# Performance work log

Measured on AMD Instinct MI355X. Metric: run time of the kernel, lower is better.

## Reference

```python
import jax, jax.numpy as jnp
import numpy as np

B_SZ = 8
G = 2048
D_MODEL = 512
D_STATE = 128
D_CONV = 4
EXPAND = 2
HEADDIM = 64
D_INNER = EXPAND * D_MODEL          # 1024
NHEADS = D_INNER // HEADDIM         # 16
CONV_DIM = D_INNER + 2 * D_STATE    # 1280
D_IN_PROJ = 2 * D_INNER + 2 * D_STATE + NHEADS  # 2320
ID_DIM = 128
CHR_DIM = 64
N_CHR = 25
F_LOCUS = 32
PATH_DIM = 128
GENE_FEAT = ID_DIM + PATH_DIM + 2 * CHR_DIM  # 384
N_PERT = 10000
P_DIM = 128


def silu(x):
    return x * jax.nn.sigmoid(x)


def causal_dw_conv(x, w, b):
    # x: (B,L,C), w: (C,K), b: (C,)  causal depthwise conv (left pad K-1)
    K = w.shape[1]
    L = x.shape[1]
    xp = jnp.pad(x, ((0, 0), (K - 1, 0), (0, 0)))
    out = b[None, None, :]
    for k in range(K):
        out = out + xp[:, k:k + L, :] * w[:, k][None, None, :]
    return out


def mamba2(u, in_w, conv_w, conv_b, dt_bias, A_log, Dp, norm_w, out_w):
    # u: (B,L,d_model) -> (B,L,d_model); mamba_ssm Mamba2 defaults, ngroups=1
    Bb, L, _ = u.shape
    zxbcdt = u @ in_w.T                                   # (B,L,D_IN_PROJ)
    z = zxbcdt[..., :D_INNER]
    xBC = zxbcdt[..., D_INNER:D_INNER + CONV_DIM]
    dt = zxbcdt[..., D_INNER + CONV_DIM:]                 # (B,L,H)
    xBC = silu(causal_dw_conv(xBC, conv_w, conv_b))
    x = xBC[..., :D_INNER].reshape(Bb, L, NHEADS, HEADDIM)
    Bm = xBC[..., D_INNER:D_INNER + D_STATE]              # (B,L,N)
    Cm = xBC[..., D_INNER + D_STATE:]                     # (B,L,N)
    dt = jax.nn.softplus(dt + dt_bias)                    # (B,L,H)
    dA = jnp.exp(dt * (-jnp.exp(A_log)))                  # (B,L,H)

    def step(h, inp):
        dA_t, dt_t, B_t, C_t, x_t = inp
        h = dA_t[:, :, None, None] * h + jnp.einsum('bh,bn,bhp->bhpn', dt_t, B_t, x_t)
        y = jnp.einsum('bhpn,bn->bhp', h, C_t)
        return h, y

    h0 = jnp.zeros((Bb, NHEADS, HEADDIM, D_STATE), u.dtype)
    xs = (dA.transpose(1, 0, 2), dt.transpose(1, 0, 2),
          Bm.transpose(1, 0, 2), Cm.transpose(1, 0, 2), x.transpose(1, 0, 2, 3))
    _, ys = jax.lax.scan(step, h0, xs)                    # ys: (L,B,H,P)
    y = ys.transpose(1, 0, 2, 3) + Dp[None, None, :, None] * x
    y = y.reshape(Bb, L, D_INNER)
    # gated RMSNorm (norm_before_gate=False): norm(y * silu(z))
    y = y * silu(z)
    y = y * jax.lax.rsqrt(jnp.mean(y * y, axis=-1, keepdims=True) + 1e-5) * norm_w
    return y @ out_w.T


def setup_inputs() -> dict:
    key = jax.random.key(0)
    ks = iter(jax.random.split(key, 48))

    def nrm(shape, scale):
        return jax.random.normal(next(ks), shape, jnp.float32) * scale

    inp = {}
    inp['perturbation_idx'] = jax.random.randint(next(ks), (B_SZ,), 0, N_PERT)
    inp['chr_idx'] = jax.random.randint(next(ks), (G,), 0, N_CHR)
    inp['locus_fourier'] = nrm((G, 2 * F_LOCUS), 1.0)
    inp['pathway_features'] = nrm((G, PATH_DIM), 1.0)
    inp['pert_emb'] = nrm((N_PERT, P_DIM), 0.02)
    inp['gene_id_emb'] = nrm((G, ID_DIM), 0.02)
    inp['chr_emb'] = nrm((N_CHR, CHR_DIM), 0.02)
    inp['locus_w'] = nrm((CHR_DIM, 2 * F_LOCUS), (2 * F_LOCUS) ** -0.5)
    inp['locus_b'] = jnp.zeros((CHR_DIM,), jnp.float32)
    inp['cond_w'] = nrm((GENE_FEAT, P_DIM), P_DIM ** -0.5)
    inp['cond_b'] = jnp.zeros((GENE_FEAT,), jnp.float32)
    inp['in_w'] = nrm((D_MODEL, GENE_FEAT), GENE_FEAT ** -0.5)
    inp['in_b'] = jnp.zeros((D_MODEL,), jnp.float32)
    inp['head_w'] = nrm((1, D_MODEL), D_MODEL ** -0.5)
    inp['head_b'] = jnp.zeros((1,), jnp.float32)
    for p in ('f_', 'b_'):
        inp[p + 'in_w'] = nrm((D_IN_PROJ, D_MODEL), D_MODEL ** -0.5)
        inp[p + 'conv_w'] = nrm((CONV_DIM, D_CONV), D_CONV ** -0.5)
        inp[p + 'conv_b'] = jnp.zeros((CONV_DIM,), jnp.float32)
        inp[p + 'dt_bias'] = nrm((NHEADS,), 0.5)
        inp[p + 'A_log'] = jnp.log(jax.random.uniform(next(ks), (NHEADS,), jnp.float32, 1.0, 16.0))
        inp[p + 'D'] = jnp.ones((NHEADS,), jnp.float32)
        inp[p + 'norm_w'] = jnp.ones((D_INNER,), jnp.float32)
        inp[p + 'out_w'] = nrm((D_MODEL, D_INNER), D_INNER ** -0.5)
    return inp


def reference(perturbation_idx, chr_idx, locus_fourier, pathway_features,
              pert_emb, gene_id_emb, chr_emb, locus_w, locus_b,
              cond_w, cond_b, in_w, in_b, head_w, head_b,
              f_in_w, f_conv_w, f_conv_b, f_dt_bias, f_A_log, f_D, f_norm_w, f_out_w,
              b_in_w, b_conv_w, b_conv_b, b_dt_bias, b_A_log, b_D, b_norm_w, b_out_w):
    B = perturbation_idx.shape[0]
    cond = pert_emb[perturbation_idx] @ cond_w.T + cond_b          # (B, GENE_FEAT)
    e_chr = chr_emb[chr_idx]                                        # (G, CHR_DIM)
    e_locus = jax.nn.gelu(locus_fourier @ locus_w.T + locus_b, approximate=False)
    gene_feat = jnp.concatenate([gene_id_emb, pathway_features, e_chr, e_locus], axis=1)  # (G, GENE_FEAT)
    seq = jnp.concatenate([cond[:, None, :],
                           jnp.broadcast_to(gene_feat[None], (B,) + gene_feat.shape)], axis=1)
    seq = seq @ in_w.T + in_b                                       # (B, G+1, d_model)
    h_fwd = mamba2(seq, f_in_w, f_conv_w, f_conv_b, f_dt_bias, f_A_log, f_D, f_norm_w, f_out_w)
    h_bwd = jnp.flip(mamba2(jnp.flip(seq, axis=1), b_in_w, b_conv_w, b_conv_b,
                            b_dt_bias, b_A_log, b_D, b_norm_w, b_out_w), axis=1)
    H = h_fwd + h_bwd
    return H[:, 1:, :] @ head_w.T + head_b                          # (B, G, 1)
```

## Files before the change

### kernel.cpp

```cpp
#include <hip/hip_runtime.h>
#include <hip/hip_bf16.h>
#include <hip/hip_fp16.h>
#include <math.h>

#define DPROJ 2320
#define CONVD 1280

typedef __attribute__((ext_vector_type(8))) short bf16x8;
typedef __attribute__((ext_vector_type(4))) float f32x4;

__device__ __forceinline__ float siluf(float x) { return x / (1.f + __expf(-x)); }
__device__ __forceinline__ float bfu(unsigned short s) { return __uint_as_float(((unsigned)s) << 16); }
__device__ __forceinline__ unsigned short f2bf(float f) {
    unsigned u = __float_as_uint(f);
    unsigned r = (u + 0x7FFFu + ((u >> 16) & 1u)) >> 16;
    return (unsigned short)r;
}
__device__ __forceinline__ unsigned short f2h(float f) {
    __half h = __float2half(f);
    return *(unsigned short*)&h;
}
__device__ __forceinline__ float h2f(unsigned short s) {
    __half h = *(__half*)&s;
    return __half2float(h);
}


__global__ void gg_kernel(const int* __restrict__ chridx, const float* __restrict__ gid,
                          const float* __restrict__ path, const float* __restrict__ chrE,
                          const int* __restrict__ pidx, const float* __restrict__ pertE,
                          float* __restrict__ gf, float* __restrict__ cemb,
                          float* __restrict__ wf2, float* __restrict__ wb2) {
    int blk = blockIdx.x, tid = threadIdx.x;
    if (blk < 3072) {
        int idx = blk * 256 + tid;
        int g = idx / 384, j = idx % 384;
        float v;
        if (j < 128)      v = gid[(size_t)g * 128 + j];
        else if (j < 256) v = path[(size_t)g * 128 + (j - 128)];
        else if (j < 320) v = chrE[(size_t)chridx[g] * 64 + (j - 256)];
        else return;
        gf[idx] = v;
    } else if (blk < 3076) {
        int idx = (blk - 3072) * 256 + tid;
        int b = idx >> 7, k = idx & 127;
        cemb[idx] = pertE[(size_t)pidx[b] * 128 + k];
    } else {
        wf2[tid * 4 + 0] = 0.f; wf2[tid * 4 + 1] = 0.f;
        wf2[tid * 4 + 2] = 0.f; wf2[tid * 4 + 3] = 0.f;
        wb2[tid * 4 + 0] = 0.f; wb2[tid * 4 + 1] = 0.f;
        wb2[tid * 4 + 2] = 0.f; wb2[tid * 4 + 3] = 0.f;
    }
}

__global__ void wfold_kernel(const float* __restrict__ headW,
                             const float* __restrict__ fOutW, const float* __restrict__ fNw,
                             const float* __restrict__ bOutW, const float* __restrict__ bNw,
                             float* __restrict__ wf2, float* __restrict__ wb2) {
    int blk = blockIdx.x;
    int dir = blk >> 6;
    int rem = blk & 63;
    int dseg = rem >> 4, mseg = rem & 15;
    int tid = threadIdx.x;
    int d = dseg * 256 + tid;
    const float* W = dir ? bOutW : fOutW;
    float s = 0.f;
#pragma unroll
    for (int m = mseg * 32; m < mseg * 32 + 32; ++m)
        s += headW[m] * W[(size_t)m * 1024 + d];
    const float* nw = dir ? bNw : fNw;
    atomicAdd(&(dir ? wb2 : wf2)[d], s * nw[d]);
}


__global__ void tobf4_kernel(const float* __restrict__ inW, const float* __restrict__ fInW,
                             const float* __restrict__ bInW, const float* __restrict__ gf,
                             unsigned short* __restrict__ inW2, unsigned short* __restrict__ fInW2,
                             unsigned short* __restrict__ bInW2, unsigned short* __restrict__ gf2) {
    size_t idx = (size_t)blockIdx.x * 256 + threadIdx.x;
    const size_t A = 512UL * 384, B5 = 2432UL * 512;
    if (idx < A) {
        inW2[idx] = f2bf(inW[idx]);
    } else if (idx < A + B5) {
        size_t k = idx - A; int m = k / 512, kk = k % 512;
        fInW2[k] = f2bf(m < 2320 ? fInW[(size_t)m * 512 + kk] : 0.f);
    } else if (idx < A + 2 * B5) {
        size_t k = idx - A - B5; int m = k / 512, kk = k % 512;
        bInW2[k] = f2bf(m < 2320 ? bInW[(size_t)m * 512 + kk] : 0.f);
    } else {
        size_t k = idx - A - 2 * B5;
        gf2[k] = f2bf(gf[k]);
    }
}


__global__ __launch_bounds__(256) void mfma_gemm_kernel(
    const unsigned short* __restrict__ A2, const unsigned short* __restrict__ W2,
    const float* __restrict__ bias,
    unsigned short* __restrict__ Cbf, unsigned short* __restrict__ sz,
    unsigned short* __restrict__ xbc, float* __restrict__ dtr,
    int N, int K2, int ldc) {
    __shared__ __align__(16) unsigned short Al[128 * 40];
    __shared__ __align__(16) unsigned short Bl[128 * 40];
    const int tid = threadIdx.x;
    const int bm = blockIdx.y * 128, bn = blockIdx.x * 128;
    const int lane = tid & 63, wave = tid >> 6;
    const int wm = (wave >> 1) * 64, wn = (wave & 1) * 64;
    f32x4 acc[4][4];
#pragma unroll
    for (int i = 0; i < 4; ++i)
#pragma unroll
        for (int j = 0; j < 4; ++j) acc[i][j] = (f32x4){0.f, 0.f, 0.f, 0.f};

    for (int k0 = 0; k0 < K2; k0 += 32) {
        __syncthreads();
#pragma unroll
        for (int s = 0; s < 2; ++s) {
            int ch = tid + 256 * s;
            int row = ch >> 2, q = ch & 3;
            uint4 va = *(const uint4*)&A2[(size_t)(bm + row) * K2 + k0 + q * 8];
            *(uint4*)&Al[row * 40 + q * 8] = va;
            uint4 vb = *(const uint4*)&W2[(size_t)(bn + row) * K2 + k0 + q * 8];
            *(uint4*)&Bl[row * 40 + q * 8] = vb;
        }
        __syncthreads();
        bf16x8 af[4], bfr[4];
#pragma unroll
        for (int i = 0; i < 4; ++i)
            af[i] = *(const bf16x8*)&Al[(wm + i * 16 + (lane & 15)) * 40 + (lane >> 4) * 8];
#pragma unroll
        for (int j = 0; j < 4; ++j)
            bfr[j] = *(const bf16x8*)&Bl[(wn + j * 16 + (lane & 15)) * 40 + (lane >> 4) * 8];
#pragma unroll
        for (int i = 0; i < 4; ++i)
#pragma unroll
            for (int j = 0; j < 4; ++j)
                acc[i][j] = __builtin_amdgcn_mfma_f32_16x16x32_bf16(af[i], bfr[j], acc[i][j], 0, 0, 0);
    }
#pragma unroll
    for (int i = 0; i < 4; ++i) {
        int m = bm + wm + i * 16 + (lane >> 4) * 4;
#pragma unroll
        for (int j = 0; j < 4; ++j) {
            int n = bn + wn + j * 16 + (lane & 15);
            if (n < N) {
                float bv = bias ? bias[n] : 0.f;
#pragma unroll
                for (int r = 0; r < 4; ++r) {
                    float v = acc[i][j][r] + bv;
                    if (Cbf) {
                        Cbf[(size_t)(m + r) * ldc + n] = f2bf(v);
                    } else if (n < 1024) {
                        sz[(size_t)(m + r) * 1024 + n] = f2h(siluf(v));
                    } else if (n < 2304) {
                        xbc[(size_t)(m + r) * 1280 + (n - 1024)] = f2bf(v);
                    } else {
                        dtr[(size_t)(m + r) * 16 + (n - 2304)] = v;
                    }
                }
            }
        }
    }
}


__global__ __launch_bounds__(256) void gemm_kernel(
    const float* __restrict__ A, const float* __restrict__ W,
    const float* __restrict__ bias, float* __restrict__ C,
    int M, int N, int K, int ldc, int act) {
    __shared__ __align__(16) float As[16][68];
    __shared__ __align__(16) float Ws[16][68];
    const int tid = threadIdx.x;
    const int tx = tid & 15, ty = tid >> 4;
    const int bm = blockIdx.y * 64, bn = blockIdx.x * 64;
    const int lr = tid >> 2;
    const int lk = (tid & 3) * 4;
    float acc[4][4];
#pragma unroll
    for (int i = 0; i < 4; ++i)
#pragma unroll
        for (int j = 0; j < 4; ++j) acc[i][j] = 0.f;

    for (int k0 = 0; k0 < K; k0 += 16) {
        const int am = bm + lr;
        const int wn = bn + lr;
        float4 av = make_float4(0.f, 0.f, 0.f, 0.f), wv = make_float4(0.f, 0.f, 0.f, 0.f);
        if (am < M) av = *(const float4*)&A[(size_t)am * K + k0 + lk];
        if (wn < N) wv = *(const float4*)&W[(size_t)wn * K + k0 + lk];
        __syncthreads();
        As[lk + 0][lr] = av.x; As[lk + 1][lr] = av.y; As[lk + 2][lr] = av.z; As[lk + 3][lr] = av.w;
        Ws[lk + 0][lr] = wv.x; Ws[lk + 1][lr] = wv.y; Ws[lk + 2][lr] = wv.z; Ws[lk + 3][lr] = wv.w;
        __syncthreads();
#pragma unroll
        for (int kk = 0; kk < 16; ++kk) {
            float4 a = *(const float4*)&As[kk][ty * 4];
            float4 w = *(const float4*)&Ws[kk][tx * 4];
            float aa[4] = {a.x, a.y, a.z, a.w}, ww[4] = {w.x, w.y, w.z, w.w};
#pragma unroll
            for (int i = 0; i < 4; ++i)
#pragma unroll
                for (int j = 0; j < 4; ++j) acc[i][j] += aa[i] * ww[j];
        }
    }
#pragma unroll
    for (int i = 0; i < 4; ++i) {
        const int m = bm + ty * 4 + i;
        if (m >= M) continue;
#pragma unroll
        for (int j = 0; j < 4; ++j) {
            const int n = bn + tx * 4 + j;
            if (n >= N) continue;
            float v = acc[i][j] + (bias ? bias[n] : 0.f);
            if (act == 1) v = 0.5f * v * (1.f + erff(v * 0.70710678118654752f));
            C[(size_t)m * ldc + n] = v;
        }
    }
}


__global__ void dt_kernel(const float* __restrict__ dtrF, const float* __restrict__ dtrB,
                          const float* __restrict__ zxc,
                          const float* __restrict__ fDtB, const float* __restrict__ bDtB,
                          float* __restrict__ dtFsT, float* __restrict__ dtBsT,
                          float* __restrict__ dtFp) {
    int idx = blockIdx.x * 256 + threadIdx.x;
    if (idx < 32768) {
        int r = idx >> 4, hh = idx & 15;
        float raw = dtrF[idx] + fDtB[hh];
        dtFsT[hh * 2048 + r] = (raw > 20.f) ? raw : log1pf(expf(raw));
    } else if (idx < 65536) {
        int k = idx - 32768;
        int r = k >> 4, hh = k & 15;
        float raw = dtrB[(size_t)(2047 - r) * 16 + hh] + bDtB[hh];
        dtBsT[hh * 2048 + r] = (raw > 20.f) ? raw : log1pf(expf(raw));
    } else if (idx < 65664) {
        int k = idx - 65536;
        int b = k >> 4, hh = k & 15;
        float raw = zxc[(size_t)b * DPROJ + 2304 + hh] + fDtB[hh];
        dtFp[k] = (raw > 20.f) ? raw : log1pf(expf(raw));
    }
}
// ... 194 lines not shown
            for (int r = 0; r < 4; ++r) {
                int t = tm + i * 16 + quad * 4 + r;
                float v = (s <= t) ? __expf(scum[t] - cs) * ds * acc1[i][j][r] : 0.f;
                Sm[t * 72 + s] = f2bf(v);
            }
        }
    }
    __syncthreads();

    const int pm = (wave >> 1) * 32, tn = (wave & 1) * 32;
    f32x4 acc2[2][2];
#pragma unroll
    for (int i = 0; i < 2; ++i)
#pragma unroll
        for (int j = 0; j < 2; ++j) acc2[i][j] = (f32x4){0.f, 0.f, 0.f, 0.f};
#pragma unroll
    for (int ks = 0; ks < 2; ++ks) {
        bf16x8 af[2], bfr[2];
#pragma unroll
        for (int i = 0; i < 2; ++i)
            af[i] = *(const bf16x8*)&XT[(pm + i * 16 + l15) * 72 + ks * 32 + quad * 8];
#pragma unroll
        for (int j = 0; j < 2; ++j)
            bfr[j] = *(const bf16x8*)&Sm[(tn + j * 16 + l15) * 72 + ks * 32 + quad * 8];
#pragma unroll
        for (int i = 0; i < 2; ++i)
#pragma unroll
            for (int j = 0; j < 2; ++j)
                acc2[i][j] = __builtin_amdgcn_mfma_f32_16x16x32_bf16(af[i], bfr[j], acc2[i][j], 0, 0, 0);
    }
#pragma unroll
    for (int i = 0; i < 2; ++i)
#pragma unroll
        for (int j = 0; j < 2; ++j) {
            int t = tn + j * 16 + l15;
            int p0 = pm + i * 16 + quad * 4;
            ushort4 o = make_ushort4(f2bf(acc2[i][j][0]), f2bf(acc2[i][j][1]),
                                     f2bf(acc2[i][j][2]), f2bf(acc2[i][j][3]));
            *(ushort4*)&Yout[t * 64 + p0] = o;
        }

    const int nm = wave * 32;
    f32x4 acc3[2][4];
#pragma unroll
    for (int i = 0; i < 2; ++i)
#pragma unroll
        for (int j = 0; j < 4; ++j) acc3[i][j] = (f32x4){0.f, 0.f, 0.f, 0.f};
#pragma unroll
    for (int ks = 0; ks < 2; ++ks) {
        float ev[8];
#pragma unroll
        for (int jj = 0; jj < 8; ++jj) ev[jj] = se[ks * 32 + quad * 8 + jj];
        bf16x8 bfx[4];
#pragma unroll
        for (int j = 0; j < 4; ++j) {
            bf16x8 xs = *(const bf16x8*)&XT[(j * 16 + l15) * 72 + ks * 32 + quad * 8];
#pragma unroll
            for (int jj = 0; jj < 8; ++jj)
                bfx[j][jj] = (short)f2bf(bfu((unsigned short)xs[jj]) * ev[jj]);
        }
        bf16x8 af[2];
#pragma unroll
        for (int i = 0; i < 2; ++i)
            af[i] = *(const bf16x8*)&BT[(nm + i * 16 + l15) * 72 + ks * 32 + quad * 8];
#pragma unroll
        for (int i = 0; i < 2; ++i)
#pragma unroll
            for (int j = 0; j < 4; ++j)
                acc3[i][j] = __builtin_amdgcn_mfma_f32_16x16x32_bf16(af[i], bfx[j], acc3[i][j], 0, 0, 0);
    }
#pragma unroll
    for (int i = 0; i < 2; ++i)
#pragma unroll
        for (int j = 0; j < 4; ++j) {
            int p = j * 16 + l15;
            int n0 = nm + i * 16 + quad * 4;
            ushort4 o = make_ushort4(f2bf(acc3[i][j][0]), f2bf(acc3[i][j][1]),
                                     f2bf(acc3[i][j][2]), f2bf(acc3[i][j][3]));
            *(ushort4*)&Uout[p * 128 + n0] = o;
        }
}


__global__ void cbm_kernel(const float* __restrict__ convFp, const unsigned short* __restrict__ bcF,
                           const float* __restrict__ dtFp, const float* __restrict__ cumF,
                           const unsigned short* __restrict__ UF0,
                           float* __restrict__ cb0, unsigned short* __restrict__ Mb) {
    int blk = blockIdx.x, tid = threadIdx.x;
    if (blk < 32) {
        int idx = blk * 256 + tid;
        int b = idx >> 10, r = idx & 1023, h = r >> 6, tl = r & 63;
        int t = tl + 1;
        const float* b0 = convFp + (size_t)(b * 4) * CONVD;
        float s = 0.f;
        if (t < 4) {
            const float* crow = convFp + (size_t)(b * 4 + t) * CONVD;
            for (int n = 0; n < 128; ++n) s += crow[1152 + n] * b0[1024 + n];
        } else {
            const unsigned short* cr = bcF + (size_t)(t - 4) * 256 + 128;
            for (int n = 0; n < 128; ++n) s += bfu(cr[n]) * b0[1024 + n];
        }
        cb0[(b * 16 + h) * 64 + tl] = s * dtFp[b * 16 + h];
    } else {
        int bh = blk - 32;
        int b = bh >> 4, h = bh & 15;
        float D0 = __expf(cumF[h * 2048 + 63]);
        float dt0 = dtFp[b * 16 + h];
        const float* row0 = convFp + (size_t)(b * 4) * CONVD;
        const unsigned short* u = UF0 + (size_t)(b * 16 + h) * 8192;
        unsigned short* m = Mb + (size_t)(b * 16 + h) * 8192;
        for (int e4 = tid; e4 < 2048; e4 += 256) {
            int e = e4 * 4, p = e >> 7, n0 = e & 127;
            float s = D0 * dt0 * row0[h * 64 + p];
            float4 B4 = *(const float4*)&row0[1024 + n0];
            ushort4 uv = *(const ushort4*)&u[e];
            ushort4 o = make_ushort4(f2bf(s * B4.x + bfu(uv.x)), f2bf(s * B4.y + bfu(uv.y)),
                                     f2bf(s * B4.z + bfu(uv.z)), f2bf(s * B4.w + bfu(uv.w)));
            *(ushort4*)&m[e] = o;
        }
    }
}


__global__ void tpsi_kernel(const unsigned short* __restrict__ UFs, const unsigned short* __restrict__ UB,
                            const float* __restrict__ cumF, const float* __restrict__ cumB,
                            unsigned short* __restrict__ Tst, float* __restrict__ psiF) {
    int blk = blockIdx.x;
    int dir = blk >> 7, h = (blk >> 3) & 15, q8 = blk & 7;
    int tid = threadIdx.x;
    const unsigned short* U = dir ? UB : UFs;
    const float* cum = dir ? cumB : cumF;
    unsigned short* T = Tst + (size_t)(dir * 16 + h) * 32 * 8192;
    if (dir == 0 && q8 == 0 && tid == 0) {
        float ps = 1.f;
        for (int c = 1; c < 32; ++c) {
            psiF[h * 32 + c] = ps;
            ps *= __expf(cumF[h * 2048 + c * 64 + 63]);
        }
    }
    const size_t e = (size_t)q8 * 1024 + 4 * tid;
    float4 st = make_float4(0.f, 0.f, 0.f, 0.f);
    const int c0 = dir ? 0 : 1;
    ushort4 u = *(const ushort4*)&U[((size_t)c0 * 16 + h) * 8192 + e];
    for (int c = c0; c < 32; ++c) {
        ushort4 un = make_ushort4(0, 0, 0, 0);
        if (c + 1 < 32) un = *(const ushort4*)&U[((size_t)(c + 1) * 16 + h) * 8192 + e];
        float Dc = __expf(cum[h * 2048 + c * 64 + 63]);
        ushort4 o = make_ushort4(f2bf(st.x), f2bf(st.y), f2bf(st.z), f2bf(st.w));
        *(ushort4*)&T[(size_t)c * 8192 + e] = o;
        st.x = Dc * st.x + bfu(u.x);
        st.y = Dc * st.y + bfu(u.y);
        st.z = Dc * st.z + bfu(u.z);
        st.w = Dc * st.w + bfu(u.w);
        u = un;
    }
}


__global__ __launch_bounds__(256) void yt_kernel(
    const unsigned short* __restrict__ bcF, const unsigned short* __restrict__ bcB,
    const unsigned short* __restrict__ Tst,
    unsigned short* __restrict__ YtF, unsigned short* __restrict__ YtB) {
    const int iid = blockIdx.x;
    int dir, h, c;
    if (iid < 496) { dir = 0; c = 1 + (iid >> 4); h = iid & 15; }
    else           { int k = iid - 496; dir = 1; c = k >> 4; h = k & 15; }
    const unsigned short* Cbase = (dir == 0)
        ? bcF + ((size_t)(64 * c - 3)) * 256 + 128
        : bcB + ((size_t)(64 * c)) * 256 + 128;
    const unsigned short* Tp = Tst + ((size_t)(dir * 16 + h) * 32 + c) * 8192;
    unsigned short* Yt = (dir == 0 ? YtF : YtB) + (size_t)(c * 16 + h) * 4096;
    const int tid = threadIdx.x;
    const int lane = tid & 63, wave = tid >> 6;
    const int quad = lane >> 4, l15 = lane & 15;
    const int pm = (wave >> 1) * 32, tb = (wave & 1) * 32;
    f32x4 acc[2][2];
#pragma unroll
    for (int i = 0; i < 2; ++i)
#pragma unroll
        for (int j = 0; j < 2; ++j) acc[i][j] = (f32x4){0.f, 0.f, 0.f, 0.f};
#pragma unroll
    for (int ks = 0; ks < 4; ++ks) {
        bf16x8 af[2], bfr[2];
#pragma unroll
        for (int i = 0; i < 2; ++i)
            af[i] = *(const bf16x8*)&Tp[(size_t)(pm + i * 16 + l15) * 128 + ks * 32 + quad * 8];
#pragma unroll
        for (int j = 0; j < 2; ++j)
            bfr[j] = *(const bf16x8*)&Cbase[(size_t)(tb + j * 16 + l15) * 256 + ks * 32 + quad * 8];
#pragma unroll
        for (int i = 0; i < 2; ++i)
#pragma unroll
            for (int j = 0; j < 2; ++j)
                acc[i][j] = __builtin_amdgcn_mfma_f32_16x16x32_bf16(af[i], bfr[j], acc[i][j], 0, 0, 0);
    }
#pragma unroll
    for (int i = 0; i < 2; ++i)
#pragma unroll
        for (int j = 0; j < 2; ++j) {
            int t = tb + j * 16 + l15;
            int p0 = pm + i * 16 + quad * 4;
            ushort4 o = make_ushort4(f2bf(acc[i][j][0]), f2bf(acc[i][j][1]),
                                     f2bf(acc[i][j][2]), f2bf(acc[i][j][3]));
            *(ushort4*)&Yt[t * 64 + p0] = o;
        }
}


__global__ __launch_bounds__(256) void gate_kernel(
    const unsigned short* __restrict__ bcF,
    const unsigned short* __restrict__ Mb, const float* __restrict__ psiF,
    const unsigned short* __restrict__ YtF, const unsigned short* __restrict__ YtB,
    const unsigned short* __restrict__ xF16, const unsigned short* __restrict__ xFp16,
    const unsigned short* __restrict__ xB16,
    const unsigned short* __restrict__ szF, const unsigned short* __restrict__ szB,
    const float* __restrict__ convFp,
    const float* __restrict__ cumF, const float* __restrict__ cumB,
    const unsigned short* __restrict__ YiF0, const unsigned short* __restrict__ YiFs,
    const unsigned short* __restrict__ YiB,
    const float* __restrict__ cb0,
    const float* __restrict__ fD, const float* __restrict__ bD,
    const float* __restrict__ wf2, const float* __restrict__ wb2,
    float* __restrict__ aF, float* __restrict__ aB) {
    __shared__ __align__(16) float Ysm[64 * 68];

    const int iid = blockIdx.x;
    int dir, b = 0, h, cg;
    if (iid < 1024) { dir = 0; b = iid >> 7; int r = iid & 127; h = r >> 3; cg = r & 7; }
    else            { int k = iid - 1024; dir = 1; h = k >> 3; cg = k & 7; }
    const int tid = threadIdx.x, tx = tid & 15, ty = tid >> 4;
    const int lane = tid & 63, wave = tid >> 6;
    const int quad = lane >> 4, l15 = lane & 15;

    const float Dh = (dir ? bD : fD)[h];
    const float* wvp = dir ? wb2 : wf2;
    float4 wreg = *(const float4*)&wvp[h * 64 + tx * 4];
    const float* cumA = dir ? cumB : cumF;

    const int pm = (wave >> 1) * 32, tb = (wave & 1) * 32;
    bf16x8 mfr[4][2];
    if (dir == 0) {
        const unsigned short* Mp = Mb + (size_t)(b * 16 + h) * 8192;
#pragma unroll
        for (int ks = 0; ks < 4; ++ks)
#pragma unroll
            for (int i = 0; i < 2; ++i)
                mfr[ks][i] = *(const bf16x8*)&Mp[(size_t)(pm + i * 16 + l15) * 128 + ks * 32 + quad * 8];
    }

    for (int cc = 0; cc < 4; ++cc) {
        const int c = cg * 4 + cc;
        const bool fwdG = (dir == 0 && c > 0);
        if (fwdG) {
            if (cc > 0) __syncthreads();
            const unsigned short* Cbase = bcF + ((size_t)(64 * c - 3)) * 256 + 128;
            f32x4 acc[2][2];
#pragma unroll
            for (int i = 0; i < 2; ++i)
#pragma unroll
                for (int j = 0; j < 2; ++j) acc[i][j] = (f32x4){0.f, 0.f, 0.f, 0.f};
#pragma unroll
            for (int ks = 0; ks < 4; ++ks) {
                bf16x8 bfr[2];
#pragma unroll
                for (int j = 0; j < 2; ++j)
                    bfr[j] = *(const bf16x8*)&Cbase[(size_t)(tb + j * 16 + l15) * 256 + ks * 32 + quad * 8];
#pragma unroll
                for (int i = 0; i < 2; ++i)
#pragma unroll
                    for (int j = 0; j < 2; ++j)
                        acc[i][j] = __builtin_amdgcn_mfma_f32_16x16x32_bf16(mfr[ks][i], bfr[j], acc[i][j], 0, 0, 0);
            }
#pragma unroll
            for (int i = 0; i < 2; ++i)
#pragma unroll
                for (int j = 0; j < 2; ++j)
                    *(f32x4*)&Ysm[(tb + j * 16 + l15) * 68 + pm + i * 16 + quad * 4] = acc[i][j];
            __syncthreads();
        }

        const float psi = fwdG ? psiF[h * 32 + c] : 0.f;
        const unsigned short* Ytp = fwdG ? (YtF + (size_t)(c * 16 + h) * 4096)
                                         : (dir ? (YtB + (size_t)(c * 16 + h) * 4096) : nullptr);
        float4 x0v = make_float4(0.f, 0.f, 0.f, 0.f);
        float cbv[4] = {0.f, 0.f, 0.f, 0.f};
        if (dir == 0 && c == 0) {
            x0v = *(const float4*)&convFp[(size_t)(b * 4) * CONVD + h * 64 + tx * 4];
#pragma unroll
            for (int i = 0; i < 4; ++i) cbv[i] = cb0[(b * 16 + h) * 64 + (ty + 16 * i)];
        }

        float rawet[4];
        ushort4 yi4a[4], x4a[4], z4a[4], yt4a[4];
        float4 cm4a[4];
#pragma unroll
        for (int i = 0; i < 4; ++i) {
            int tl = ty + 16 * i;
            int j = 64 * c + tl;
            rawet[i] = cumA[h * 2048 + j];
            const unsigned short *Yi, *xp, *zp;
            if (dir == 0) {
                Yi = (c == 0) ? YiF0 + (size_t)(b * 16 + h) * 4096 : YiFs + (size_t)(c * 16 + h) * 4096;
                if (c == 0) {
                    int t = j + 1;
                    xp = (t < 4) ? xFp16 + (size_t)(b * 4 + t) * 1024 : xF16 + (size_t)(t - 4) * 1024;
                } else {
                    xp = xF16 + (size_t)(64 * c + tl - 3) * 1024;
                }
                zp = szF + (size_t)j * 1024;
            } else {
                Yi = YiB + (size_t)(c * 16 + h) * 4096;
                xp = xB16 + (size_t)j * 1024;
                zp = szB + (size_t)(2047 - j) * 1024;
            }
            yi4a[i] = *(const ushort4*)&Yi[tl * 64 + tx * 4];
            x4a[i] = *(const ushort4*)&xp[h * 64 + tx * 4];
            z4a[i] = *(const ushort4*)&zp[h * 64 + tx * 4];
            yt4a[i] = Ytp ? *(const ushort4*)&Ytp[tl * 64 + tx * 4] : make_ushort4(0, 0, 0, 0);
            cm4a[i] = fwdG ? *(const float4*)&Ysm[tl * 68 + tx * 4] : make_float4(0.f, 0.f, 0.f, 0.f);
        }

#pragma unroll
        for (int i = 0; i < 4; ++i) {
            int j = 64 * c + ty + 16 * i;
            float et = __expf(rawet[i]);
            float yv[4] = {bfu(yi4a[i].x), bfu(yi4a[i].y), bfu(yi4a[i].z), bfu(yi4a[i].w)};
            float xa[4] = {bfu(x4a[i].x), bfu(x4a[i].y), bfu(x4a[i].z), bfu(x4a[i].w)};
            float sza[4] = {h2f(z4a[i].x), h2f(z4a[i].y), h2f(z4a[i].z), h2f(z4a[i].w)};
            float ya[4] = {bfu(yt4a[i].x) + psi * cm4a[i].x, bfu(yt4a[i].y) + psi * cm4a[i].y,
                           bfu(yt4a[i].z) + psi * cm4a[i].z, bfu(yt4a[i].w) + psi * cm4a[i].w};
            float x0a[4] = {x0v.x, x0v.y, x0v.z, x0v.w};
            float wa[4] = {wreg.x, wreg.y, wreg.z, wreg.w};
            float a1 = 0.f, a2 = 0.f;
#pragma unroll
            for (int w = 0; w < 4; ++w) {
                float tot = yv[w] + et * (ya[w] + cbv[i] * x0a[w]) + Dh * xa[w];
                float g = tot * sza[w];
                a1 += g * wa[w];
                a2 += g * g;
            }
#pragma unroll
            for (int m = 1; m < 16; m <<= 1) {
                a1 += __shfl_xor(a1, m);
                a2 += __shfl_xor(a2, m);
            }
            if (tx == 0) {
                if (dir == 0) {
                    size_t o = ((size_t)(b * 2048 + j) * 16 + h) * 2;
                    aF[o] = a1; aF[o + 1] = a2;
                } else {
                    int g = 2047 - j;
                    size_t o = ((size_t)g * 16 + h) * 2;
                    aB[o] = a1; aB[o + 1] = a2;
                }
            }
        }
    }
}


__global__ void final_kernel(const float* __restrict__ aF, const float* __restrict__ aB,
                             const float* __restrict__ headB, float* __restrict__ out) {
    int idx = blockIdx.x * 256 + threadIdx.x;
    int b = idx >> 11, g = idx & 2047;
    const float* pf = aF + ((size_t)(b * 2048 + g)) * 32;
    const float* pb = aB + (size_t)g * 32;
    float f1 = 0.f, f2 = 0.f, b1 = 0.f, b2 = 0.f;
#pragma unroll
    for (int h = 0; h < 16; ++h) {
        f1 += pf[2 * h]; f2 += pf[2 * h + 1];
        b1 += pb[2 * h]; b2 += pb[2 * h + 1];
    }
    out[idx] = f1 * rsqrtf(f2 * (1.f / 1024.f) + 1e-5f) +
               b1 * rsqrtf(b2 * (1.f / 1024.f) + 1e-5f) + headB[0];
}


extern "C" void kernel_launch(void* const* d_in, const int* in_sizes, int n_in,
                              void* d_out, int out_size, void* d_ws, size_t ws_size,
                              hipStream_t stream) {
    const int*   pidx   = (const int*)  d_in[0];
    const int*   chridx = (const int*)  d_in[1];
    const float* locusF = (const float*)d_in[2];
    const float* pathF  = (const float*)d_in[3];
    const float* pertE  = (const float*)d_in[4];
    const float* gidE   = (const float*)d_in[5];
    const float* chrE   = (const float*)d_in[6];
    const float* locusW = (const float*)d_in[7];
    const float* locusB = (const float*)d_in[8];
    const float* condW  = (const float*)d_in[9];
    const float* condB  = (const float*)d_in[10];
    const float* inW    = (const float*)d_in[11];
    const float* inB    = (const float*)d_in[12];
    const float* headW  = (const float*)d_in[13];
    const float* headB  = (const float*)d_in[14];
    const float* fInW   = (const float*)d_in[15];
    const float* fCw    = (const float*)d_in[16];
    const float* fCb    = (const float*)d_in[17];
    const float* fDtB   = (const float*)d_in[18];
    const float* fAlog  = (const float*)d_in[19];
    const float* fDp    = (const float*)d_in[20];
    const float* fNw    = (const float*)d_in[21];
    const float* fOutW  = (const float*)d_in[22];
    const float* bInW   = (const float*)d_in[23];
    const float* bCw    = (const float*)d_in[24];
    const float* bCb    = (const float*)d_in[25];
    const float* bDtB   = (const float*)d_in[26];
    const float* bAlog  = (const float*)d_in[27];
    const float* bDp    = (const float*)d_in[28];
    const float* bNw    = (const float*)d_in[29];
    const float* bOutW  = (const float*)d_in[30];
    float* out = (float*)d_out;
    (void)in_sizes; (void)n_in; (void)out_size; (void)ws_size;

    char* base = (char*)d_ws;
    size_t off = 0;
    auto allocf = [&](size_t n) -> float* {
        char* r = base + off; off += ((n * 4 + 63) & ~(size_t)63); return (float*)r; };
    auto allocu = [&](size_t n) -> unsigned short* {
        char* r = base + off; off += ((n * 2 + 63) & ~(size_t)63); return (unsigned short*)r; };

    float* gf     = allocf(2048UL * 384);
    float* cond   = allocf(8UL * 384);
    float* cemb   = allocf(8UL * 128);
    float* uc     = allocf(8UL * 512);
    float* zxc    = allocf(8UL * DPROJ);
    float* convFp = allocf(8UL * 4 * CONVD);
    float* dtrF   = allocf(2048UL * 16);
    float* dtrB   = allocf(2048UL * 16);
    float* dtFsT  = allocf(16UL * 2048);
    float* dtFp   = allocf(128);
    float* dtBsT  = allocf(16UL * 2048);
    float* cumF   = allocf(16UL * 2048);
    float* cumB   = allocf(16UL * 2048);
    float* wf2    = allocf(1024);
    float* wb2    = allocf(1024);
    float* cb0    = allocf(8UL * 16 * 64);
    float* psiF   = allocf(16UL * 32);
    float* aF     = allocf(8UL * 2048 * 16 * 2);
    float* aB     = allocf(2048UL * 16 * 2);
    unsigned short* xbcF = allocu(2048UL * 1280);
    unsigned short* xbcB = allocu(2048UL * 1280);
    unsigned short* YiF0 = allocu(8UL * 16 * 4096);
    unsigned short* YiFs = allocu(32UL * 16 * 4096);
    unsigned short* YiB  = allocu(32UL * 16 * 4096);
    unsigned short* UF0  = allocu(8UL * 16 * 8192);
    unsigned short* UFs  = allocu(32UL * 16 * 8192);
    unsigned short* UB   = allocu(32UL * 16 * 8192);
    unsigned short* Mb   = allocu(8UL * 16 * 8192);
    unsigned short* Tst  = allocu(2UL * 16 * 32 * 8192);
    unsigned short* bcF  = allocu(2045UL * 256);
    unsigned short* bcFp = allocu(32UL * 256);
    unsigned short* bcB  = allocu(2048UL * 256);
    unsigned short* YtF  = allocu(32UL * 16 * 4096);
    unsigned short* YtB  = allocu(32UL * 16 * 4096);
    unsigned short* xF16 = allocu(2045UL * 1024);
    unsigned short* xFp16= allocu(32UL * 1024);
    unsigned short* xB16 = allocu(2048UL * 1024);
    unsigned short* szF  = allocu(2048UL * 1024);
    unsigned short* szB  = allocu(2048UL * 1024);
    unsigned short* gf2   = allocu(2048UL * 384);
    unsigned short* inW2  = allocu(512UL * 384);
    unsigned short* ug2   = allocu(2048UL * 512);
    unsigned short* fInW2 = allocu(2432UL * 512);
    unsigned short* bInW2 = allocu(2432UL * 512);

    gg_kernel<<<3077, 256, 0, stream>>>(chridx, gidE, pathF, chrE, pidx, pertE, gf, cemb, wf2, wb2);
    wfold_kernel<<<128, 256, 0, stream>>>(headW, fOutW, fNw, bOutW, bNw, wf2, wb2);
    gemm_kernel<<<dim3(1, 32), 256, 0, stream>>>(locusF, locusW, locusB, gf + 320, 2048, 64, 64, 384, 1);
    gemm_kernel<<<dim3(6, 1), 256, 0, stream>>>(cemb, condW, condB, cond, 8, 384, 128, 384, 0);

    tobf4_kernel<<<13568, 256, 0, stream>>>(inW, fInW, bInW, gf, inW2, fInW2, bInW2, gf2);

    mfma_gemm_kernel<<<dim3(4, 16), 256, 0, stream>>>(gf2, inW2, inB, ug2, nullptr, nullptr, nullptr, 512, 384, 512);
    gemm_kernel<<<dim3(8, 1), 256, 0, stream>>>(cond, inW, inB, uc, 8, 512, 384, 512, 0);

    mfma_gemm_kernel<<<dim3(19, 16), 256, 0, stream>>>(ug2, fInW2, nullptr, nullptr, szF, xbcF, dtrF, 2320, 512, 0);
    mfma_gemm_kernel<<<dim3(19, 16), 256, 0, stream>>>(ug2, bInW2, nullptr, nullptr, szB, xbcB, dtrB, 2320, 512, 0);
    gemm_kernel<<<dim3(37, 1), 256, 0, stream>>>(uc, fInW, nullptr, zxc, 8, DPROJ, 512, DPROJ, 0);

    dt_kernel<<<257, 256, 0, stream>>>(dtrF, dtrB, zxc, fDtB, bDtB, dtFsT, dtBsT, dtFp);
    cum_kernel<<<4, 256, 0, stream>>>(dtFsT, dtBsT, fAlog, bAlog, cumF, cumB);
    conv_kernel<<<20625, 256, 0, stream>>>(xbcF, xbcB, zxc, fCw, fCb, bCw, bCb,
                                           bcF, xF16, bcB, xB16, convFp, bcFp, xFp16);
    intra_kernel<<<1136, 256, 0, stream>>>(bcF, bcFp, bcB, xF16, xFp16, xB16,
                                           dtFsT, dtBsT, cumF, cumB,
                                           YiF0, YiFs, YiB, UF0, UFs, UB);
    cbm_kernel<<<160, 256, 0, stream>>>(convFp, bcF, dtFp, cumF, UF0, cb0, Mb);
    tpsi_kernel<<<256, 256, 0, stream>>>(UFs, UB, cumF, cumB, Tst, psiF);
    yt_kernel<<<1008, 256, 0, stream>>>(bcF, bcB, Tst, YtF, YtB);
    gate_kernel<<<1152, 256, 0, stream>>>(bcF, Mb, psiF, YtF, YtB, xF16, xFp16, xB16,
                                          szF, szB, convFp, cumF, cumB,
                                          YiF0, YiFs, YiB, cb0, fDp, bDp, wf2, wb2, aF, aB);
    final_kernel<<<64, 256, 0, stream>>>(aF, aB, headB, out);
}
```

Measured before the change: 389.2 us.

## Merge fwd/bwd in-proj GEMMs, fuse cbm+tpsi, fold intra-chunk Y into yt

The two direction-specific in-projection GEMM launches become one launch with a doubled grid that selects weights and outputs by block index. The cbm and tpsi kernels merge into a single mid_kernel launch. The yt kernel now adds the intra-chunk Y and applies the exp(cum) decay itself, so the gate kernel reads one combined Y tensor instead of two and does less per-element work. This cuts launch count and gate-kernel memory traffic, but yt now does extra reads and adds one more bf16 rounding of the summed value.

```diff
diff --git a/kernel.cpp b/kernel.cpp
--- a/kernel.cpp
+++ b/kernel.cpp
@@ -96,9 +96,7 @@
 
 __global__ __launch_bounds__(256) void mfma_gemm_kernel(
     const unsigned short* __restrict__ A2, const unsigned short* __restrict__ W2,
-    const float* __restrict__ bias,
-    unsigned short* __restrict__ Cbf, unsigned short* __restrict__ sz,
-    unsigned short* __restrict__ xbc, float* __restrict__ dtr,
+    const float* __restrict__ bias, unsigned short* __restrict__ Cbf,
     int N, int K2, int ldc) {
     __shared__ __align__(16) unsigned short Al[128 * 40];
     __shared__ __align__(16) unsigned short Bl[128 * 40];
@@ -146,17 +144,79 @@
             if (n < N) {
                 float bv = bias ? bias[n] : 0.f;
 #pragma unroll
+                for (int r = 0; r < 4; ++r)
+                    Cbf[(size_t)(m + r) * ldc + n] = f2bf(acc[i][j][r] + bv);
+            }
+        }
+    }
+}
+
+
+__global__ __launch_bounds__(256) void zx_gemm_kernel(
+    const unsigned short* __restrict__ A2,
+    const unsigned short* __restrict__ fInW2, const unsigned short* __restrict__ bInW2,
+    unsigned short* __restrict__ szF, unsigned short* __restrict__ xbcF, float* __restrict__ dtrF,
+    unsigned short* __restrict__ szB, unsigned short* __restrict__ xbcB, float* __restrict__ dtrB) {
+    __shared__ __align__(16) unsigned short Al[128 * 40];
+    __shared__ __align__(16) unsigned short Bl[128 * 40];
+    const int tid = threadIdx.x;
+    const int bxx = blockIdx.x;
+    const int d = (bxx >= 19);
+    const int bn = (d ? bxx - 19 : bxx) * 128, bm = blockIdx.y * 128;
+    const unsigned short* W2 = d ? bInW2 : fInW2;
+    unsigned short* sz = d ? szB : szF;
+    unsigned short* xbc = d ? xbcB : xbcF;
+    float* dtr = d ? dtrB : dtrF;
+    const int lane = tid & 63, wave = tid >> 6;
+    const int wm = (wave >> 1) * 64, wn = (wave & 1) * 64;
+    const int K2 = 512, N = 2320;
+    f32x4 acc[4][4];
+#pragma unroll
+    for (int i = 0; i < 4; ++i)
+#pragma unroll
+        for (int j = 0; j < 4; ++j) acc[i][j] = (f32x4){0.f, 0.f, 0.f, 0.f};
+
+    for (int k0 = 0; k0 < K2; k0 += 32) {
+        __syncthreads();
+#pragma unroll
+        for (int s = 0; s < 2; ++s) {
+            int ch = tid + 256 * s;
+            int row = ch >> 2, q = ch & 3;
+            uint4 va = *(const uint4*)&A2[(size_t)(bm + row) * K2 + k0 + q * 8];
+            *(uint4*)&Al[row * 40 + q * 8] = va;
+            uint4 vb = *(const uint4*)&W2[(size_t)(bn + row) * K2 + k0 + q * 8];
+            *(uint4*)&Bl[row * 40 + q * 8] = vb;
+        }
+        __syncthreads();
+        bf16x8 af[4], bfr[4];
+#pragma unroll
+        for (int i = 0; i < 4; ++i)
+            af[i] = *(const bf16x8*)&Al[(wm + i * 16 + (lane & 15)) * 40 + (lane >> 4) * 8];
+#pragma unroll
+        for (int j = 0; j < 4; ++j)
+            bfr[j] = *(const bf16x8*)&Bl[(wn + j * 16 + (lane & 15)) * 40 + (lane >> 4) * 8];
+#pragma unroll
+        for (int i = 0; i < 4; ++i)
+#pragma unroll
+            for (int j = 0; j < 4; ++j)
+                acc[i][j] = __builtin_amdgcn_mfma_f32_16x16x32_bf16(af[i], bfr[j], acc[i][j], 0, 0, 0);
+    }
+#pragma unroll
+    for (int i = 0; i < 4; ++i) {
+        int m = bm + wm + i * 16 + (lane >> 4) * 4;
+#pragma unroll
+        for (int j = 0; j < 4; ++j) {
+            int n = bn + wn + j * 16 + (lane & 15);
+            if (n < N) {
+#pragma unroll
                 for (int r = 0; r < 4; ++r) {
-                    float v = acc[i][j][r] + bv;
-                    if (Cbf) {
-                        Cbf[(size_t)(m + r) * ldc + n] = f2bf(v);
-                    } else if (n < 1024) {
+                    float v = acc[i][j][r];
+                    if (n < 1024)
                         sz[(size_t)(m + r) * 1024 + n] = f2h(siluf(v));
-                    } else if (n < 2304) {
+                    else if (n < 2304)
                         xbc[(size_t)(m + r) * 1280 + (n - 1024)] = f2bf(v);
-                    } else {
+                    else
                         dtr[(size_t)(m + r) * 16 + (n - 2304)] = v;
-                    }
                 }
             }
         }
@@ -517,10 +577,13 @@
 }
 
 
-__global__ void cbm_kernel(const float* __restrict__ convFp, const unsigned short* __restrict__ bcF,
+__global__ void mid_kernel(const float* __restrict__ convFp, const unsigned short* __restrict__ bcF,
                            const float* __restrict__ dtFp, const float* __restrict__ cumF,
+                           const float* __restrict__ cumB,
                            const unsigned short* __restrict__ UF0,
-                           float* __restrict__ cb0, unsigned short* __restrict__ Mb) {
+                           const unsigned short* __restrict__ UFs, const unsigned short* __restrict__ UB,
+                           float* __restrict__ cb0, unsigned short* __restrict__ Mb,
+                           unsigned short* __restrict__ Tst, float* __restrict__ psiF) {
     int blk = blockIdx.x, tid = threadIdx.x;
     if (blk < 32) {
         int idx = blk * 256 + tid;
@@ -536,7 +599,7 @@
             for (int n = 0; n < 128; ++n) s += bfu(cr[n]) * b0[1024 + n];
         }
         cb0[(b * 16 + h) * 64 + tl] = s * dtFp[b * 16 + h];
-    } else {
+    } else if (blk < 160) {
         int bh = blk - 32;
         int b = bh >> 4, h = bh & 15;
         float D0 = __expf(cumF[h * 2048 + 63]);
@@ -553,41 +616,35 @@
                                      f2bf(s * B4.z + bfu(uv.z)), f2bf(s * B4.w + bfu(uv.w)));
             *(ushort4*)&m[e] = o;
         }
-    }
-}
-
-
-__global__ void tpsi_kernel(const unsigned short* __restrict__ UFs, const unsigned short* __restrict__ UB,
-                            const float* __restrict__ cumF, const float* __restrict__ cumB,
-                            unsigned short* __restrict__ Tst, float* __restrict__ psiF) {
-    int blk = blockIdx.x;
-    int dir = blk >> 7, h = (blk >> 3) & 15, q8 = blk & 7;
-    int tid = threadIdx.x;
-    const unsigned short* U = dir ? UB : UFs;
-    const float* cum = dir ? cumB : cumF;
-    unsigned short* T = Tst + (size_t)(dir * 16 + h) * 32 * 8192;
-    if (dir == 0 && q8 == 0 && tid == 0) {
-        float ps = 1.f;
-        for (int c = 1; c < 32; ++c) {
-            psiF[h * 32 + c] = ps;
-            ps *= __expf(cumF[h * 2048 + c * 64 + 63]);
-        }
-    }
-    const size_t e = (size_t)q8 * 1024 + 4 * tid;
-    float4 st = make_float4(0.f, 0.f, 0.f, 0.f);
-    const int c0 = dir ? 0 : 1;
-    ushort4 u = *(const ushort4*)&U[((size_t)c0 * 16 + h) * 8192 + e];
-    for (int c = c0; c < 32; ++c) {
-        ushort4 un = make_ushort4(0, 0, 0, 0);
-        if (c + 1 < 32) un = *(const ushort4*)&U[((size_t)(c + 1) * 16 + h) * 8192 + e];
-        float Dc = __expf(cum[h * 2048 + c * 64 + 63]);
-        ushort4 o = make_ushort4(f2bf(st.x), f2bf(st.y), f2bf(st.z), f2bf(st.w));
-        *(ushort4*)&T[(size_t)c * 8192 + e] = o;
-        st.x = Dc * st.x + bfu(u.x);
-        st.y = Dc * st.y + bfu(u.y);
-        st.z = Dc * st.z + bfu(u.z);
-        st.w = Dc * st.w + bfu(u.w);
-        u = un;
+    } else {
+        int blk2 = blk - 160;
+        int dir = blk2 >> 7, h = (blk2 >> 3) & 15, q8 = blk2 & 7;
+        const unsigned short* U = dir ? UB : UFs;
+        const float* cum = dir ? cumB : cumF;
+        unsigned short* T = Tst + (size_t)(dir * 16 + h) * 32 * 8192;
+        if (dir == 0 && q8 == 0 && tid == 0) {
+            float ps = 1.f;
+            for (int c = 1; c < 32; ++c) {
+                psiF[h * 32 + c] = ps;
+                ps *= __expf(cumF[h * 2048 + c * 64 + 63]);
+            }
+        }
+        const size_t e = (size_t)q8 * 1024 + 4 * tid;
+        float4 st = make_float4(0.f, 0.f, 0.f, 0.f);
+        const int c0 = dir ? 0 : 1;
+        ushort4 u = *(const ushort4*)&U[((size_t)c0 * 16 + h) * 8192 + e];
+        for (int c = c0; c < 32; ++c) {
+            ushort4 un = make_ushort4(0, 0, 0, 0);
+            if (c + 1 < 32) un = *(const ushort4*)&U[((size_t)(c + 1) * 16 + h) * 8192 + e];
+            float Dc = __expf(cum[h * 2048 + c * 64 + 63]);
+            ushort4 o = make_ushort4(f2bf(st.x), f2bf(st.y), f2bf(st.z), f2bf(st.w));
+            *(ushort4*)&T[(size_t)c * 8192 + e] = o;
+            st.x = Dc * st.x + bfu(u.x);
+            st.y = Dc * st.y + bfu(u.y);
+            st.z = Dc * st.z + bfu(u.z);
+            st.w = Dc * st.w + bfu(u.w);
+            u = un;
+        }
     }
 }
 
@@ -595,7 +652,9 @@
 __global__ __launch_bounds__(256) void yt_kernel(
     const unsigned short* __restrict__ bcF, const unsigned short* __restrict__ bcB,
     const unsigned short* __restrict__ Tst,
-    unsigned short* __restrict__ YtF, unsigned short* __restrict__ YtB) {
+    const unsigned short* __restrict__ YiFs, const unsigned short* __restrict__ YiB,
+    const float* __restrict__ cumF, const float* __restrict__ cumB,
+    unsigned short* __restrict__ YsF, unsigned short* __restrict__ YsB) {
     const int iid = blockIdx.x;
     int dir, h, c;
     if (iid < 496) { dir = 0; c = 1 + (iid >> 4); h = iid & 15; }
@@ -604,7 +663,9 @@
         ? bcF + ((size_t)(64 * c - 3)) * 256 + 128
         : bcB + ((size_t)(64 * c)) * 256 + 128;
     const unsigned short* Tp = Tst + ((size_t)(dir * 16 + h) * 32 + c) * 8192;
-    unsigned short* Yt = (dir == 0 ? YtF : YtB) + (size_t)(c * 16 + h) * 4096;
+    const unsigned short* Yi = (dir == 0 ? YiFs : YiB) + (size_t)(c * 16 + h) * 4096;
+    const float* cum = dir ? cumB : cumF;
+    unsigned short* Ys = (dir == 0 ? YsF : YsB) + (size_t)(c * 16 + h) * 4096;
     const int tid = threadIdx.x;
     const int lane = tid & 63, wave = tid >> 6;
     const int quad = lane >> 4, l15 = lane & 15;
@@ -635,9 +696,13 @@
         for (int j = 0; j < 2; ++j) {
             int t = tb + j * 16 + l15;
             int p0 = pm + i * 16 + quad * 4;
-            ushort4 o = make_ushort4(f2bf(acc[i][j][0]), f2bf(acc[i][j][1]),
-                                     f2bf(acc[i][j][2]), f2bf(acc[i][j][3]));
-            *(ushort4*)&Yt[t * 64 + p0] = o;
+            float et = __expf(cum[h * 2048 + 64 * c + t]);
+            ushort4 yi = *(const ushort4*)&Yi[t * 64 + p0];
+            ushort4 o = make_ushort4(f2bf(bfu(yi.x) + et * acc[i][j][0]),
+                                     f2bf(bfu(yi.y) + et * acc[i][j][1]),
+                                     f2bf(bfu(yi.z) + et * acc[i][j][2]),
+                                     f2bf(bfu(yi.w) + et * acc[i][j][3]));
+            *(ushort4*)&Ys[t * 64 + p0] = o;
         }
 }
 
@@ -645,14 +710,13 @@
 __global__ __launch_bounds__(256) void gate_kernel(
     const unsigned short* __restrict__ bcF,
     const unsigned short* __restrict__ Mb, const float* __restrict__ psiF,
-    const unsigned short* __restrict__ YtF, const unsigned short* __restrict__ YtB,
+    const unsigned short* __restrict__ YsF, const unsigned short* __restrict__ YsB,
     const unsigned short* __restrict__ xF16, const unsigned short* __restrict__ xFp16,
     const unsigned short* __restrict__ xB16,
     const unsigned short* __restrict__ szF, const unsigned short* __restrict__ szB,
     const float* __restrict__ convFp,
-    const float* __restrict__ cumF, const float* __restrict__ cumB,
-    const unsigned short* __restrict__ YiF0, const unsigned short* __restrict__ YiFs,
-    const unsigned short* __restrict__ YiB,
+    const float* __restrict__ cumF,
+    const unsigned short* __restrict__ YiF0,
     const float* __restrict__ cb0,
     const float* __restrict__ fD, const float* __restrict__ bD,
     const float* __restrict__ wf2, const float* __restrict__ wb2,
@@ -670,7 +734,6 @@
     const float Dh = (dir ? bD : fD)[h];
     const float* wvp = dir ? wb2 : wf2;
     float4 wreg = *(const float4*)&wvp[h * 64 + tx * 4];
-    const float* cumA = dir ? cumB : cumF;
 
     const int pm = (wave >> 1) * 32, tb = (wave & 1) * 32;
     bf16x8 mfr[4][2];
@@ -715,8 +778,6 @@
         }
 
         const float psi = fwdG ? psiF[h * 32 + c] : 0.f;
-        const unsigned short* Ytp = fwdG ? (YtF + (size_t)(c * 16 + h) * 4096)
-                                         : (dir ? (YtB + (size_t)(c * 16 + h) * 4096) : nullptr);
         float4 x0v = make_float4(0.f, 0.f, 0.f, 0.f);
         float cbv[4] = {0.f, 0.f, 0.f, 0.f};
         if (dir == 0 && c == 0) {
@@ -726,16 +787,16 @@
         }
 
         float rawet[4];
-        ushort4 yi4a[4], x4a[4], z4a[4], yt4a[4];
+        ushort4 y4a[4], x4a[4], z4a[4];
         float4 cm4a[4];
 #pragma unroll
         for (int i = 0; i < 4; ++i) {
             int tl = ty + 16 * i;
             int j = 64 * c + tl;
-            rawet[i] = cumA[h * 2048 + j];
-            const unsigned short *Yi, *xp, *zp;
+            rawet[i] = (dir == 0) ? cumF[h * 2048 + j] : 0.f;
+            const unsigned short *Yp, *xp, *zp;
             if (dir == 0) {
-                Yi = (c == 0) ? YiF0 + (size_t)(b * 16 + h) * 4096 : YiFs + (size_t)(c * 16 + h) * 4096;
+                Yp = (c == 0) ? YiF0 + (size_t)(b * 16 + h) * 4096 : YsF + (size_t)(c * 16 + h) * 4096;
                 if (c == 0) {
                     int t = j + 1;
                     xp = (t < 4) ? xFp16 + (size_t)(b * 4 + t) * 1024 : xF16 + (size_t)(t - 4) * 1024;
@@ -744,32 +805,35 @@
                 }
                 zp = szF + (size_t)j * 1024;
             } else {
-                Yi = YiB + (size_t)(c * 16 + h) * 4096;
+                Yp = YsB + (size_t)(c * 16 + h) * 4096;
                 xp = xB16 + (size_t)j * 1024;
                 zp = szB + (size_t)(2047 - j) * 1024;
             }
-            yi4a[i] = *(const ushort4*)&Yi[tl * 64 + tx * 4];
+            y4a[i] = *(const ushort4*)&Yp[tl * 64 + tx * 4];
             x4a[i] = *(const ushort4*)&xp[h * 64 + tx * 4];
             z4a[i] = *(const ushort4*)&zp[h * 64 + tx * 4];
-            yt4a[i] = Ytp ? *(const ushort4*)&Ytp[tl * 64 + tx * 4] : make_ushort4(0, 0, 0, 0);
-            cm4a[i] = fwdG ? *(const float4*)&Ysm[tl * 68 + tx * 4] : make_float4(0.f, 0.f, 0.f, 0.f);
+            if (fwdG)                    cm4a[i] = *(const float4*)&Ysm[tl * 68 + tx * 4];
+            else if (dir == 0 && c == 0) cm4a[i] = x0v;
+            else                         cm4a[i] = make_float4(0.f, 0.f, 0.f, 0.f);
         }
 
 #pragma unroll
         for (int i = 0; i < 4; ++i) {
             int j = 64 * c + ty + 16 * i;
-            float et = __expf(rawet[i]);
-            float yv[4] = {bfu(yi4a[i].x), bfu(yi4a[i].y), bfu(yi4a[i].z), bfu(yi4a[i].w)};
+            float k1 = 0.f;
+            if (dir == 0) {
+                float et = __expf(rawet[i]);
+                k1 = (c == 0) ? et * cbv[i] : et * psi;
+            }
+            float yv[4] = {bfu(y4a[i].x), bfu(y4a[i].y), bfu(y4a[i].z), bfu(y4a[i].w)};
             float xa[4] = {bfu(x4a[i].x), bfu(x4a[i].y), bfu(x4a[i].z), bfu(x4a[i].w)};
             float sza[4] = {h2f(z4a[i].x), h2f(z4a[i].y), h2f(z4a[i].z), h2f(z4a[i].w)};
-            float ya[4] = {bfu(yt4a[i].x) + psi * cm4a[i].x, bfu(yt4a[i].y) + psi * cm4a[i].y,
-                           bfu(yt4a[i].z) + psi * cm4a[i].z, bfu(yt4a[i].w) + psi * cm4a[i].w};
-            float x0a[4] = {x0v.x, x0v.y, x0v.z, x0v.w};
+            float cma[4] = {cm4a[i].x, cm4a[i].y, cm4a[i].z, cm4a[i].w};
             float wa[4] = {wreg.x, wreg.y, wreg.z, wreg.w};
             float a1 = 0.f, a2 = 0.f;
 #pragma unroll
             for (int w = 0; w < 4; ++w) {
-                float tot = yv[w] + et * (ya[w] + cbv[i] * x0a[w]) + Dh * xa[w];
+                float tot = yv[w] + k1 * cma[w] + Dh * xa[w];
                 float g = tot * sza[w];
                 a1 += g * wa[w];
                 a2 += g * g;
@@ -887,8 +951,8 @@
     unsigned short* bcF  = allocu(2045UL * 256);
     unsigned short* bcFp = allocu(32UL * 256);
     unsigned short* bcB  = allocu(2048UL * 256);
-    unsigned short* YtF  = allocu(32UL * 16 * 4096);
-    unsigned short* YtB  = allocu(32UL * 16 * 4096);
+    unsigned short* YsF  = allocu(32UL * 16 * 4096);
+    unsigned short* YsB  = allocu(32UL * 16 * 4096);
     unsigned short* xF16 = allocu(2045UL * 1024);
     unsigned short* xFp16= allocu(32UL * 1024);
     unsigned short* xB16 = allocu(2048UL * 1024);
@@ -907,11 +971,11 @@
 
     tobf4_kernel<<<13568, 256, 0, stream>>>(inW, fInW, bInW, gf, inW2, fInW2, bInW2, gf2);
 
-    mfma_gemm_kernel<<<dim3(4, 16), 256, 0, stream>>>(gf2, inW2, inB, ug2, nullptr, nullptr, nullptr, 512, 384, 512);
+    mfma_gemm_kernel<<<dim3(4, 16), 256, 0, stream>>>(gf2, inW2, inB, ug2, 512, 384, 512);
     gemm_kernel<<<dim3(8, 1), 256, 0, stream>>>(cond, inW, inB, uc, 8, 512, 384, 512, 0);
 
-    mfma_gemm_kernel<<<dim3(19, 16), 256, 0, stream>>>(ug2, fInW2, nullptr, nullptr, szF, xbcF, dtrF, 2320, 512, 0);
-    mfma_gemm_kernel<<<dim3(19, 16), 256, 0, stream>>>(ug2, bInW2, nullptr, nullptr, szB, xbcB, dtrB, 2320, 512, 0);
+    zx_gemm_kernel<<<dim3(38, 16), 256, 0, stream>>>(ug2, fInW2, bInW2,
+                                                     szF, xbcF, dtrF, szB, xbcB, dtrB);
     gemm_kernel<<<dim3(37, 1), 256, 0, stream>>>(uc, fInW, nullptr, zxc, 8, DPROJ, 512, DPROJ, 0);
 
     dt_kernel<<<257, 256, 0, stream>>>(dtrF, dtrB, zxc, fDtB, bDtB, dtFsT, dtBsT, dtFp);
@@ -921,11 +985,11 @@
     intra_kernel<<<1136, 256, 0, stream>>>(bcF, bcFp, bcB, xF16, xFp16, xB16,
                                            dtFsT, dtBsT, cumF, cumB,
                                            YiF0, YiFs, YiB, UF0, UFs, UB);
-    cbm_kernel<<<160, 256, 0, stream>>>(convFp, bcF, dtFp, cumF, UF0, cb0, Mb);
-    tpsi_kernel<<<256, 256, 0, stream>>>(UFs, UB, cumF, cumB, Tst, psiF);
-    yt_kernel<<<1008, 256, 0, stream>>>(bcF, bcB, Tst, YtF, YtB);
-    gate_kernel<<<1152, 256, 0, stream>>>(bcF, Mb, psiF, YtF, YtB, xF16, xFp16, xB16,
-                                          szF, szB, convFp, cumF, cumB,
-                                          YiF0, YiFs, YiB, cb0, fDp, bDp, wf2, wb2, aF, aB);
+    mid_kernel<<<416, 256, 0, stream>>>(convFp, bcF, dtFp, cumF, cumB, UF0, UFs, UB,
+                                        cb0, Mb, Tst, psiF);
+    yt_kernel<<<1008, 256, 0, stream>>>(bcF, bcB, Tst, YiFs, YiB, cumF, cumB, YsF, YsB);
+    gate_kernel<<<1152, 256, 0, stream>>>(bcF, Mb, psiF, YsF, YsB, xF16, xFp16, xB16,
+                                          szF, szB, convFp, cumF,
+                                          YiF0, cb0, fDp, bDp, wf2, wb2, aF, aB);
     final_kernel<<<64, 256, 0, stream>>>(aF, aB, headB, out);
 }
```

Result: faster. 372.9 us (-4.2%).
